# Optimization experiments

Hardware: AMD Instinct MI355X
Metric: run time of the kernel (lower is better)

The kernel has to match this reference:

```python
import jax, jax.numpy as jnp
import numpy as np

# Standard 24-joint SMPL kinematic tree
PARENTS = [-1, 0, 0, 0, 1, 2, 3, 4, 5, 6, 7, 8, 9, 9, 9, 12, 13, 14, 16, 17, 18, 19, 20, 21]
NUM_JOINTS = len(PARENTS)
FEAT = 6           # local_feature_size
HID = 1 + FEAT     # n_features = bone_dim + bone_feature_dim = 7
B = 500_000


def _topo_order(parents):
    children = {i: [] for i in range(len(parents))}
    roots = []
    for i, p in enumerate(parents):
        if p == -1:
            roots.append(i)
        else:
            children[p].append(i)
    order, queue = [], roots[:]
    while queue:
        cur = queue.pop(0)
        order.append(cur)
        queue.extend(sorted(children[cur]))
    return order

TOPO = _topo_order(PARENTS)


def setup_inputs() -> dict:
    key = jax.random.key(0)
    kx, k1, k2, k3, k4 = jax.random.split(key, 5)
    x = jax.random.normal(kx, (B, NUM_JOINTS), dtype=jnp.float32)
    # Packed per-joint MLP params. For root joints only W1[:, 0] is used
    # (parent slot is fed zeros), matching the in_features=1 root BoneMLP.
    s1 = 1.0 / np.sqrt(HID)   # kaiming-uniform-like scale for Linear(7 -> 7)
    s2 = 1.0 / np.sqrt(HID)   # Linear(7 -> 6)
    W1 = jax.random.uniform(k1, (NUM_JOINTS, HID, HID), jnp.float32, -s1, s1)
    b1 = jax.random.uniform(k2, (NUM_JOINTS, HID), jnp.float32, -s1, s1)
    W2 = jax.random.uniform(k3, (NUM_JOINTS, FEAT, HID), jnp.float32, -s2, s2)
    b2 = jax.random.uniform(k4, (NUM_JOINTS, FEAT), jnp.float32, -s2, s2)
    return {"x": x, "W1": W1, "b1": b1, "W2": W2, "b2": b2}


def reference(x, W1, b1, W2, b2):
    # x: [B, 24]. Sequential topological traversal over 24 joints (fixed small
    # tree loop; the data dim B stays fully vectorized).
    zeros_parent = jnp.zeros((x.shape[0], FEAT), dtype=x.dtype)
    features = [None] * NUM_JOINTS
    for i in TOPO:
        parent = PARENTS[i]
        pf = zeros_parent if parent == -1 else features[parent]
        inp = jnp.concatenate([x[:, i, None], pf], axis=-1)      # [B, 7]
        h = jax.nn.relu(inp @ W1[i].T + b1[i])                    # [B, 7]
        features[i] = jax.nn.relu(h @ W2[i].T + b2[i])            # [B, 6]
    return jnp.concatenate(features, axis=-1)                     # [B, 144]
```

## Files before the change

kernel.cpp:

```cpp
#include <hip/hip_runtime.h>

#define NJ 24
#define HIDN 7
#define FEATN 6

__global__ __launch_bounds__(256)
void structure_encoder_kernel(const float* __restrict__ x,
                              const float* __restrict__ W1,
                              const float* __restrict__ b1,
                              const float* __restrict__ W2,
                              const float* __restrict__ b2,
                              float* __restrict__ out, int B)
{
    int row = blockIdx.x * blockDim.x + threadIdx.x;
    if (row >= B) return;

    float xv[NJ];
    const float4* xp = reinterpret_cast<const float4*>(x + (size_t)row * NJ);
    #pragma unroll
    for (int q = 0; q < 6; ++q) {
        float4 t = xp[q];
        xv[q * 4 + 0] = t.x; xv[q * 4 + 1] = t.y;
        xv[q * 4 + 2] = t.z; xv[q * 4 + 3] = t.w;
    }

    float feat[NJ][FEATN];
    float4* orow4 = reinterpret_cast<float4*>(out + (size_t)row * (NJ * FEATN));

    constexpr int parents[NJ] = {-1,0,0,0,1,2,3,4,5,6,7,8,9,9,9,12,13,14,16,17,18,19,20,21};

    #pragma unroll
    for (int j = 0; j < NJ; ++j) {
        const float* W1j = W1 + j * (HIDN * HIDN);
        const float* b1j = b1 + j * HIDN;
        const float* W2j = W2 + j * (FEATN * HIDN);
        const float* b2j = b2 + j * FEATN;

        float inp[HIDN];
        inp[0] = xv[j];
        const int p = parents[j];
        #pragma unroll
        for (int c = 0; c < FEATN; ++c)
            inp[1 + c] = (p < 0) ? 0.f : feat[p][c];

        float h[HIDN];
        #pragma unroll
        for (int r = 0; r < HIDN; ++r) {
            float acc = b1j[r];
            #pragma unroll
            for (int c = 0; c < HIDN; ++c)
                acc = fmaf(W1j[r * HIDN + c], inp[c], acc);
            h[r] = fmaxf(acc, 0.f);
        }

        #pragma unroll
        for (int r = 0; r < FEATN; ++r) {
            float acc = b2j[r];
            #pragma unroll
            for (int c = 0; c < HIDN; ++c)
                acc = fmaf(W2j[r * HIDN + c], h[c], acc);
            feat[j][r] = fmaxf(acc, 0.f);
        }

        if (j == 7 || j == 15 || j == 23) {
            const int burst = (j - 7) / 8;
            #pragma unroll
            for (int q = 0; q < 12; ++q) {
                const int f0 = burst * 48 + q * 4;
                float4 v;
                v.x = feat[(f0 + 0) / FEATN][(f0 + 0) % FEATN];
                v.y = feat[(f0 + 1) / FEATN][(f0 + 1) % FEATN];
                v.z = feat[(f0 + 2) / FEATN][(f0 + 2) % FEATN];
                v.w = feat[(f0 + 3) / FEATN][(f0 + 3) % FEATN];
                orow4[burst * 12 + q] = v;
            }
        }
    }
}

extern "C" void kernel_launch(void* const* d_in, const int* in_sizes, int n_in,
                              void* d_out, int out_size, void* d_ws, size_t ws_size,
                              hipStream_t stream) {
    const float* x  = (const float*)d_in[0];
    const float* W1 = (const float*)d_in[1];
    const float* b1 = (const float*)d_in[2];
    const float* W2 = (const float*)d_in[3];
    const float* b2 = (const float*)d_in[4];
    float* out = (float*)d_out;

    const int B = in_sizes[0] / NJ;
    const int block = 256;
    const int grid = (B + block - 1) / block;
    structure_encoder_kernel<<<grid, block, 0, stream>>>(x, W1, b1, W2, b2, out, B);
}
```

Before: 465.6 us.

## Stage input loads and output stores through per-wavefront LDS for coalescing

Each wavefront now cooperatively loads its 64 rows of x as contiguous float4s into a shared-memory tile, and each lane reads back its own row. Output bursts are written the same way: each lane puts its 12 float4s into an LDS tile padded to a stride of 13, then the wave writes them out as contiguous float4s. This targets the strided per-thread global accesses (576-byte row stride on stores), which scatter each store instruction across many cache lines. In exchange it uses about 53KB of LDS per block, which may limit occupancy. It also relies on wavefront-synchronous execution because there is no explicit barrier between the LDS writes and reads.

Result: faster. 409.4 us (-12.1%).

```diff
diff --git a/kernel.cpp b/kernel.cpp
--- a/kernel.cpp
+++ b/kernel.cpp
@@ -12,20 +12,35 @@
                               const float* __restrict__ b2,
                               float* __restrict__ out, int B)
 {
-    int row = blockIdx.x * blockDim.x + threadIdx.x;
-    if (row >= B) return;
+    __shared__ float4 obuf[4][64 * 13];
 
+    const int tid  = threadIdx.x;
+    const int wv   = tid >> 6;
+    const int lane = tid & 63;
+    float4* buf = obuf[wv];
+
+    const long long rowBase = (long long)blockIdx.x * 256 + (long long)wv * 64;
+
+    const float4* x4 = reinterpret_cast<const float4*>(x);
+    const long long xMax = (long long)B * 6 - 1;
+    #pragma unroll
+    for (int k = 0; k < 6; ++k) {
+        const int lo = lane + 64 * k;
+        long long g = rowBase * 6 + lo;
+        if (g > xMax) g = xMax;
+        const float4 v = x4[g];
+        const int r = lo / 6, s = lo - 6 * r;
+        buf[r * 13 + s] = v;
+    }
     float xv[NJ];
-    const float4* xp = reinterpret_cast<const float4*>(x + (size_t)row * NJ);
     #pragma unroll
-    for (int q = 0; q < 6; ++q) {
-        float4 t = xp[q];
-        xv[q * 4 + 0] = t.x; xv[q * 4 + 1] = t.y;
-        xv[q * 4 + 2] = t.z; xv[q * 4 + 3] = t.w;
+    for (int s = 0; s < 6; ++s) {
+        const float4 v = buf[lane * 13 + s];
+        xv[4*s+0] = v.x; xv[4*s+1] = v.y; xv[4*s+2] = v.z; xv[4*s+3] = v.w;
     }
 
     float feat[NJ][FEATN];
-    float4* orow4 = reinterpret_cast<float4*>(out + (size_t)row * (NJ * FEATN));
+    float4* out4 = reinterpret_cast<float4*>(out);
 
     constexpr int parents[NJ] = {-1,0,0,0,1,2,3,4,5,6,7,8,9,9,9,12,13,14,16,17,18,19,20,21};
 
@@ -52,7 +67,6 @@
                 acc = fmaf(W1j[r * HIDN + c], inp[c], acc);
             h[r] = fmaxf(acc, 0.f);
         }
-
         #pragma unroll
         for (int r = 0; r < FEATN; ++r) {
             float acc = b2j[r];
@@ -63,16 +77,22 @@
         }
 
         if (j == 7 || j == 15 || j == 23) {
-            const int burst = (j - 7) / 8;
+            const int b = j / 8;
             #pragma unroll
             for (int q = 0; q < 12; ++q) {
-                const int f0 = burst * 48 + q * 4;
                 float4 v;
-                v.x = feat[(f0 + 0) / FEATN][(f0 + 0) % FEATN];
-                v.y = feat[(f0 + 1) / FEATN][(f0 + 1) % FEATN];
-                v.z = feat[(f0 + 2) / FEATN][(f0 + 2) % FEATN];
-                v.w = feat[(f0 + 3) / FEATN][(f0 + 3) % FEATN];
-                orow4[burst * 12 + q] = v;
+                v.x = feat[b*8 + (4*q+0)/6][(4*q+0)%6];
+                v.y = feat[b*8 + (4*q+1)/6][(4*q+1)%6];
+                v.z = feat[b*8 + (4*q+2)/6][(4*q+2)%6];
+                v.w = feat[b*8 + (4*q+3)/6][(4*q+3)%6];
+                buf[lane * 13 + q] = v;
+            }
+            #pragma unroll
+            for (int k = 0; k < 12; ++k) {
+                const int o  = lane + 64 * k;
+                const int rr = o / 12, s = o - 12 * rr;
+                if (rowBase + rr < (long long)B)
+                    out4[(rowBase + rr) * 36 + b * 12 + s] = buf[rr * 13 + s];
             }
         }
     }
```
